# Kernel optimization log

Hardware: AMD Instinct MI355X
Metric: run time of the kernel (lower is better)

Reference implementation:

```python
import jax, jax.numpy as jnp
import numpy as np

N = 100_000      # nodes
E = 500_000      # bonds
DN = 128         # dim_node_embedding
DB = 64          # dim_bond_embedding
NTOK = 4         # num_bond_token
DIN = 2 * DN + 2 * DB  # 384
LEAKY = 0.001
LN_EPS = 1e-5
DIST_MAX = 20.0
STEP = 0.5


def _lrelu(v):
    return jnp.where(v >= 0, v, LEAKY * v)


def _layernorm(v, w, b):
    m = v.mean(-1, keepdims=True)
    var = ((v - m) ** 2).mean(-1, keepdims=True)
    return (v - m) / jnp.sqrt(var + LN_EPS) * w + b


def setup_inputs() -> dict:
    key = jax.random.key(0)
    ks = jax.random.split(key, 20)
    x = jax.random.normal(ks[0], (N, 3), dtype=jnp.float32) * 3.0
    pos = jax.random.normal(ks[1], (N, 3), dtype=jnp.float32)
    node_embedding = jax.random.normal(ks[2], (N, DN), dtype=jnp.float32)
    i0 = jax.random.randint(ks[3], (E,), 0, N)
    off = jax.random.randint(ks[4], (E,), 1, N)  # nonzero -> no self-bonds
    bond_index = jnp.stack([i0, (i0 + off) % N], axis=1).astype(jnp.int32)
    bond_types = jax.random.randint(ks[5], (E,), 0, NTOK).astype(jnp.int32)
    s = 0.02
    params = dict(
        bond_emb=jax.random.normal(ks[6], (NTOK, DB), dtype=jnp.float32),
        W0=jax.random.normal(ks[7], (DIN, DN), dtype=jnp.float32) * s,
        b0=jnp.zeros((DN,), jnp.float32),
        W1=jax.random.normal(ks[8], (DN, DN), dtype=jnp.float32) * s,
        b1=jnp.zeros((DN,), jnp.float32),
        ln1_w=jnp.ones((DN,), jnp.float32),
        ln1_b=jnp.zeros((DN,), jnp.float32),
        W2=jax.random.normal(ks[9], (DN, DN), dtype=jnp.float32) * s,
        b2=jnp.zeros((DN,), jnp.float32),
        ln2_w=jnp.ones((DN,), jnp.float32),
        ln2_b=jnp.zeros((DN,), jnp.float32),
        Wo=jax.random.normal(ks[10], (DN, 2), dtype=jnp.float32) * s,
        bo=jnp.zeros((2,), jnp.float32),
    )
    return dict(x=x, pos=pos, node_embedding=node_embedding,
                bond_index=bond_index, bond_types=bond_types, **params)


def reference(x, pos, node_embedding, bond_index, bond_types,
              bond_emb, W0, b0, W1, b1, ln1_w, ln1_b,
              W2, b2, ln2_w, ln2_b, Wo, bo):
    i = bond_index[:, 0]
    j = bond_index[:, 1]

    # ---- BondLength geometry ----
    diff = x[i] - x[j]                                   # [E,3]
    dist = jnp.linalg.norm(diff, axis=-1, keepdims=True)  # [E,1]
    u = diff / dist                                       # [E,3] unit j->i? (i-j)/d
    direction = jnp.stack([u, -u], axis=-1)               # [E,3,2]

    # ---- Smearing (gaussian RBF + overflow bin, normalized) ----
    offset = jnp.linspace(0.0, DIST_MAX, DB - 1, dtype=jnp.float32)  # [63]
    delta = DIST_MAX / (DB - 2)
    coeff = -0.5 / (delta * delta)
    rbf = jnp.exp(coeff * (dist - offset) ** 2)            # [E,63]
    ovf = (dist >= DIST_MAX).astype(x.dtype)               # [E,1]
    smear = jnp.concatenate([rbf, ovf], axis=-1)           # [E,64]
    smear = smear / smear.sum(axis=-1, keepdims=True)

    # ---- Edge MLP (LeakyMLP, num_layer=2, dim_end=2) ----
    feat = jnp.concatenate(
        [node_embedding[i], node_embedding[j], bond_emb[bond_types], smear],
        axis=-1)                                           # [E,384]
    h = _lrelu(feat @ W0 + b0)
    h = _lrelu(_layernorm(h @ W1 + b1, ln1_w, ln1_b))
    h = _lrelu(_layernorm(h @ W2 + b2, ln2_w, ln2_b))
    force = h @ Wo + bo                                    # [E,2]

    # ---- position update (scatter-add) ----
    update = force[:, None, :] * direction                 # [E,3,2]
    pos = pos.at[i].add(STEP * update[..., 0])
    pos = pos.at[j].add(STEP * update[..., 1])
    return pos
```

## Files before the change

kernel.cpp:

```cpp
#include <hip/hip_runtime.h>
#include <stdint.h>

#define N_EDGES 500000
#define N_NODES 100000
#define PREP_NG 2
#define TBINS 1280

typedef __attribute__((ext_vector_type(8))) short short8;
typedef __attribute__((ext_vector_type(4))) float floatx4;

__device__ __forceinline__ uint16_t f2bf(float f) {
  union { float f; uint32_t u; } cv; cv.f = f;
  uint32_t u = cv.u;
  return (uint16_t)((u + 0x7FFFu + ((u >> 16) & 1u)) >> 16);
}
__device__ __forceinline__ uint32_t pk2bf(float lo, float hi) {
  return __builtin_amdgcn_perm(__float_as_uint(hi), __float_as_uint(lo), 0x07060302u);
}
__device__ __forceinline__ uint16_t bftrunc(float f) {
  return (uint16_t)(__float_as_uint(f) >> 16);
}
__device__ __forceinline__ float bf2f_lo(uint32_t u) { return __uint_as_float(u << 16); }
__device__ __forceinline__ float bf2f_hi(uint32_t u) { return __uint_as_float(u & 0xFFFF0000u); }
__device__ __forceinline__ float lrelu(float v) { return fmaxf(v, 0.001f * v); }

__global__ void prep0_kernel(const float* __restrict__ W0, const float* __restrict__ b0,
                             const float* __restrict__ W1, const float* __restrict__ W2,
                             const float* __restrict__ bemb,
                             uint16_t* __restrict__ w0ab, uint16_t* __restrict__ w1f,
                             uint16_t* __restrict__ w2f, float* __restrict__ be0f,
                             const float* __restrict__ pos, float* __restrict__ out, int npos) {
  int id = blockIdx.x * 256 + threadIdx.x;
  if (id < 32768) {
    int f = id;
    int j = f & 7, lane = (f >> 3) & 63, ntt = (f >> 9) & 15, ks = f >> 13;
    int k = ks * 32 + (lane >> 4) * 8 + j;
    int row = (ntt < 8) ? k : (128 + k);
    int col = (ntt & 7) * 16 + (lane & 15);
    w0ab[f] = f2bf(W0[row * 128 + col]);
  } else if (id < 49152) {
    int f = id - 32768;
    int j = f & 7, lane = (f >> 3) & 63, nt = (f >> 9) & 7, ks = f >> 12;
    int k = ks * 32 + (lane >> 4) * 8 + j;
    w1f[f] = f2bf(W1[k * 128 + nt * 16 + (lane & 15)]);
  } else if (id < 65536) {
    int f = id - 49152;
    int j = f & 7, lane = (f >> 3) & 63, nt = (f >> 9) & 7, ks = f >> 12;
    int k = ks * 32 + (lane >> 4) * 8 + j;
    w2f[f] = f2bf(W2[k * 128 + nt * 16 + (lane & 15)]);
  } else if (id < 66048) {
    int t = id - 65536; int ty = t >> 7, n = t & 127;
    float s = b0[n];
    for (int kk = 0; kk < 64; ++kk) s += bemb[ty * 64 + kk] * W0[(256 + kk) * 128 + n];
    be0f[t] = s;
  } else if (id - 66048 < npos) {
    out[id - 66048] = pos[id - 66048];
  }
}

__global__ __attribute__((amdgpu_flat_work_group_size(256, 256)))
void prep_tp_kernel(const float* __restrict__ W0, const float* __restrict__ be0f,
                    uint16_t* __restrict__ T,
                    const float* __restrict__ nemb, const uint16_t* __restrict__ w0ab,
                    uint16_t* __restrict__ Pa, uint16_t* __restrict__ Pb) {
  __shared__ __align__(16) uint16_t aLds[4 * PREP_NG * 16 * 136];
  __shared__ float rbf[64];
  const int tid = threadIdx.x;

  if (blockIdx.x < TBINS) {
    int b = blockIdx.x;
    float dist = (float)b * (1.0f / 32.0f);
    const float delta = 20.0f / 62.0f;
    const float coeff = -0.5f / (delta * delta);
    if (tid < 64) {
      float v;
      if (tid < 63) { float d = dist - (float)tid * delta; v = __expf(coeff * d * d); }
      else v = (dist >= 20.0f) ? 1.0f : 0.0f;
      rbf[tid] = v;
    }
    __syncthreads();
    float sum = 0.0f;
    for (int k = 0; k < 64; ++k) sum += rbf[k];
    float rs = 1.0f / sum;
    for (int o = tid; o < 512; o += 256) {
      int ty = o >> 7, n = o & 127;
      float s = be0f[ty * 128 + n];
      for (int k = 0; k < 64; ++k) s += rbf[k] * rs * W0[(320 + k) * 128 + n];
      T[((size_t)(ty * TBINS + b)) * 128 + n] = f2bf(s);
    }
    return;
  }

  const int pblk = blockIdx.x - TBINS;
  const int lane = tid & 63;
  const int wave = tid >> 6;
  const int n15 = lane & 15;
  const int quad = lane >> 4;
  uint16_t* myA = aLds + wave * (PREP_NG * 16 * 136);
  const int base = pblk * (64 * PREP_NG) + wave * (16 * PREP_NG);

  {
    const int le = lane >> 2, sub = lane & 3;
#pragma unroll
    for (int it = 0; it < PREP_NG; ++it) {
      int r = base + it * 16 + le; if (r >= N_NODES) r = N_NODES - 1;
      const float4* src = (const float4*)(nemb + (size_t)r * 128);
#pragma unroll
      for (int g = 0; g < 4; ++g) {
        float4 a = src[sub * 8 + g * 2], b = src[sub * 8 + g * 2 + 1];
        uint4 pk;
        pk.x = pk2bf(a.x, a.y); pk.y = pk2bf(a.z, a.w);
        pk.z = pk2bf(b.x, b.y); pk.w = pk2bf(b.z, b.w);
        *(uint4*)(myA + (it * 16 + le) * 136 + sub * 32 + g * 8) = pk;
      }
    }
  }

  const short8* wfv = (const short8*)w0ab + lane;
#pragma unroll
  for (int q = 0; q < 4; ++q) {
    short8 bfr[16];
#pragma unroll
    for (int ks = 0; ks < 4; ++ks)
#pragma unroll
      for (int nq = 0; nq < 4; ++nq)
        bfr[ks * 4 + nq] = wfv[(ks * 16 + q * 4 + nq) * 64];
#pragma unroll
    for (int it = 0; it < PREP_NG; ++it) {
      floatx4 acc[4];
#pragma unroll
      for (int nq = 0; nq < 4; ++nq) acc[nq] = (floatx4){0.f, 0.f, 0.f, 0.f};
#pragma unroll
      for (int ks = 0; ks < 4; ++ks) {
        short8 a = *(const short8*)(myA + (it * 16 + n15) * 136 + ks * 32 + quad * 8);
#pragma unroll
        for (int nq = 0; nq < 4; ++nq)
          acc[nq] = __builtin_amdgcn_mfma_f32_16x16x32_bf16(a, bfr[ks * 4 + nq], acc[nq], 0, 0, 0);
      }
      uint16_t* dst = (q < 2) ? Pa : Pb;
      int cbase = ((q & 1) * 4) * 16 + n15;
#pragma unroll
      for (int nq = 0; nq < 4; ++nq) {
        int c = cbase + nq * 16;
#pragma unroll
        for (int r = 0; r < 4; ++r) {
          int row = base + it * 16 + quad * 4 + r;
          if (row < N_NODES) dst[(size_t)row * 128 + c] = bftrunc(acc[nq][r]);
        }
      }
    }
  }
}

__device__ __forceinline__ void gemm_g(const uint16_t* __restrict__ wf, const uint16_t* aRow,
                                       int lane, floatx4* acc) {
  short8 a[4];
#pragma unroll
  for (int ks = 0; ks < 4; ++ks) a[ks] = *(const short8*)(aRow + ks * 32);
  const short8* wv = (const short8*)wf + lane;
#pragma unroll
  for (int ks = 0; ks < 4; ++ks)
#pragma unroll
    for (int nt = 0; nt < 8; ++nt)
      acc[nt] = __builtin_amdgcn_mfma_f32_16x16x32_bf16(a[ks], wv[(ks * 8 + nt) * 64], acc[nt], 0, 0, 0);
}

__global__ __attribute__((amdgpu_flat_work_group_size(256, 256), amdgpu_waves_per_eu(4)))
void bond_mlp_kernel(const float* __restrict__ x,
                     const int* __restrict__ bidx, const int* __restrict__ btyp,
                     const uint16_t* __restrict__ Pa, const uint16_t* __restrict__ Pb,
                     const uint16_t* __restrict__ Tt, const uint16_t* __restrict__ w1f,
                     const uint16_t* __restrict__ w2f,
                     const float* __restrict__ b1, const float* __restrict__ ln1w,
                     const float* __restrict__ ln1b,
                     const float* __restrict__ b2, const float* __restrict__ ln2w,
                     const float* __restrict__ ln2b,
                     const float* __restrict__ Wo, const float* __restrict__ bo,
                     float* __restrict__ out) {
  __shared__ __align__(16) uint16_t hA_all[4 * 16 * 136];
  __shared__ float u_lds[64][3];
  __shared__ int ij_lds[64][2];

  const int tid = threadIdx.x;
  const int lane = tid & 63;
  const int wave = tid >> 6;
  const int n15 = lane & 15;
  const int quad = lane >> 4;

  uint16_t* hA = hA_all + wave * (16 * 136);

  {
    const int le = lane >> 2, sub = lane & 3;
    const int gr = wave * 16 + le;
    const int ge = blockIdx.x * 64 + gr;
    const bool valid = ge < N_EDGES;
    int vi = 0, vj = 0, bt = 0;
    if (valid) { vi = bidx[2 * ge]; vj = bidx[2 * ge + 1]; bt = btyp[ge]; }
    float dx, dy, dz;
    if (valid) {
      dx = x[3 * vi]     - x[3 * vj];
      dy = x[3 * vi + 1] - x[3 * vj + 1];
      dz = x[3 * vi + 2] - x[3 * vj + 2];
    } else { dx = 1.0f; dy = 0.0f; dz = 0.0f; }
    float dist = sqrtf(dx * dx + dy * dy + dz * dz);
    float rinv = 1.0f / dist;
    if (sub == 0) {
      u_lds[gr][0] = dx * rinv; u_lds[gr][1] = dy * rinv; u_lds[gr][2] = dz * rinv;
      ij_lds[gr][0] = vi; ij_lds[gr][1] = vj;
    }
    float fb = fminf(dist, 39.5f) * 32.0f;
    int bi = (int)fb;
    float w = fb - (float)bi;
    const uint4* pa = (const uint4*)(Pa + (size_t)vi * 128 + sub * 32);
    const uint4* pb = (const uint4*)(Pb + (size_t)vj * 128 + sub * 32);
    const uint16_t* trow = Tt + ((size_t)(bt * TBINS + bi)) * 128 + sub * 32;
    const uint4* t0p = (const uint4*)trow;
    const uint4* t1p = (const uint4*)(trow + 128);
#pragma unroll
    for (int g = 0; g < 4; ++g) {
      uint4 av = pa[g], bv = pb[g], t0 = t0p[g], t1 = t1p[g];
      uint4 pk;
      {
        float lo = bf2f_lo(av.x) + bf2f_lo(bv.x), hi = bf2f_hi(av.x) + bf2f_hi(bv.x);
        float l0 = bf2f_lo(t0.x), l1 = bf2f_lo(t1.x), h0 = bf2f_hi(t0.x), h1 = bf2f_hi(t1.x);
        pk.x = pk2bf(lrelu(lo + l0 + w * (l1 - l0)), lrelu(hi + h0 + w * (h1 - h0)));
      }
      {
        float lo = bf2f_lo(av.y) + bf2f_lo(bv.y), hi = bf2f_hi(av.y) + bf2f_hi(bv.y);
        float l0 = bf2f_lo(t0.y), l1 = bf2f_lo(t1.y), h0 = bf2f_hi(t0.y), h1 = bf2f_hi(t1.y);
        pk.y = pk2bf(lrelu(lo + l0 + w * (l1 - l0)), lrelu(hi + h0 + w * (h1 - h0)));
      }
      {
        float lo = bf2f_lo(av.z) + bf2f_lo(bv.z), hi = bf2f_hi(av.z) + bf2f_hi(bv.z);
        float l0 = bf2f_lo(t0.z), l1 = bf2f_lo(t1.z), h0 = bf2f_hi(t0.z), h1 = bf2f_hi(t1.z);
        pk.z = pk2bf(lrelu(lo + l0 + w * (l1 - l0)), lrelu(hi + h0 + w * (h1 - h0)));
      }
      {
        float lo = bf2f_lo(av.w) + bf2f_lo(bv.w), hi = bf2f_hi(av.w) + bf2f_hi(bv.w);
        float l0 = bf2f_lo(t0.w), l1 = bf2f_lo(t1.w), h0 = bf2f_hi(t0.w), h1 = bf2f_hi(t1.w);
        pk.w = pk2bf(lrelu(lo + l0 + w * (l1 - l0)), lrelu(hi + h0 + w * (h1 - h0)));
      }
      *(uint4*)(hA + le * 136 + sub * 32 + g * 8) = pk;
    }
  }

  const uint16_t* aRow = hA + n15 * 136 + quad * 8;

  floatx4 acc[8];
#pragma unroll
  for (int nt = 0; nt < 8; ++nt) acc[nt] = (floatx4){0.f, 0.f, 0.f, 0.f};
  gemm_g(w1f, aRow, lane, acc);

  {
    float bv[8], wv[8], bb2[8];
#pragma unroll
    for (int nt = 0; nt < 8; ++nt) {
      int col = nt * 16 + n15;
      bv[nt] = b1[col]; wv[nt] = ln1w[col]; bb2[nt] = ln1b[col];
    }
    float s[4] = {0,0,0,0}, q[4] = {0,0,0,0};
#pragma unroll
    for (int nt = 0; nt < 8; ++nt)
#pragma unroll
      for (int r = 0; r < 4; ++r) { float v = acc[nt][r] + bv[nt]; s[r] += v; q[r] += v * v; }
#pragma unroll
    for (int m = 1; m <= 8; m <<= 1)
#pragma unroll
      for (int r = 0; r < 4; ++r) { s[r] += __shfl_xor(s[r], m); q[r] += __shfl_xor(q[r], m); }
    float mean[4], rstd[4];
#pragma unroll
    for (int r = 0; r < 4; ++r) {
      mean[r] = s[r] * (1.0f / 128.0f);
      float var = q[r] * (1.0f / 128.0f) - mean[r] * mean[r];
      rstd[r] = rsqrtf(var + 1e-5f);
    }
#pragma unroll
    for (int nt = 0; nt < 8; ++nt)
#pragma unroll
      for (int r = 0; r < 4; ++r) {
        float v = acc[nt][r] + bv[nt];
        float vn = (v - mean[r]) * rstd[r] * wv[nt] + bb2[nt];
        hA[(quad * 4 + r) * 136 + nt * 16 + n15] = bftrunc(lrelu(vn));
      }
  }

#pragma unroll
  for (int nt = 0; nt < 8; ++nt) acc[nt] = (floatx4){0.f, 0.f, 0.f, 0.f};
  gemm_g(w2f, aRow, lane, acc);

  {
    float bv[8], wv[8], bb2[8], wo0[8], wo1[8];
#pragma unroll
    for (int nt = 0; nt < 8; ++nt) {
      int col = nt * 16 + n15;
      bv[nt] = b2[col]; wv[nt] = ln2w[col]; bb2[nt] = ln2b[col];
      wo0[nt] = Wo[2 * col]; wo1[nt] = Wo[2 * col + 1];
    }
    float s[4] = {0,0,0,0}, q[4] = {0,0,0,0};
#pragma unroll
    for (int nt = 0; nt < 8; ++nt)
#pragma unroll
      for (int r = 0; r < 4; ++r) { float v = acc[nt][r] + bv[nt]; s[r] += v; q[r] += v * v; }
#pragma unroll
    for (int m = 1; m <= 8; m <<= 1)
#pragma unroll
      for (int r = 0; r < 4; ++r) { s[r] += __shfl_xor(s[r], m); q[r] += __shfl_xor(q[r], m); }
    float mean[4], rstd[4];
#pragma unroll
    for (int r = 0; r < 4; ++r) {
      mean[r] = s[r] * (1.0f / 128.0f);
      float var = q[r] * (1.0f / 128.0f) - mean[r] * mean[r];
      rstd[r] = rsqrtf(var + 1e-5f);
    }
    float f0[4] = {0,0,0,0}, f1[4] = {0,0,0,0};
#pragma unroll
    for (int nt = 0; nt < 8; ++nt)
#pragma unroll
      for (int r = 0; r < 4; ++r) {
        float v = acc[nt][r] + bv[nt];
        float vn = lrelu((v - mean[r]) * rstd[r] * wv[nt] + bb2[nt]);
        f0[r] += vn * wo0[nt];
        f1[r] += vn * wo1[nt];
      }
#pragma unroll
    for (int m = 1; m <= 8; m <<= 1)
#pragma unroll
      for (int r = 0; r < 4; ++r) { f0[r] += __shfl_xor(f0[r], m); f1[r] += __shfl_xor(f1[r], m); }

    if (n15 < 4) {
      int gr = wave * 16 + quad * 4 + n15;
      int ge2 = blockIdx.x * 64 + gr;
      if (ge2 < N_EDGES) {
        float F0 = (n15 == 0) ? f0[0] : (n15 == 1) ? f0[1] : (n15 == 2) ? f0[2] : f0[3];
        float F1 = (n15 == 0) ? f1[0] : (n15 == 1) ? f1[1] : (n15 == 2) ? f1[2] : f1[3];
        F0 += bo[0]; F1 += bo[1];
        float ux = u_lds[gr][0], uy = u_lds[gr][1], uz = u_lds[gr][2];
        int ii = ij_lds[gr][0], jj = ij_lds[gr][1];
        float c0 = 0.5f * F0;
        float c1 = -0.5f * F1;
        atomicAdd(out + 3 * ii,     c0 * ux);
        atomicAdd(out + 3 * ii + 1, c0 * uy);
        atomicAdd(out + 3 * ii + 2, c0 * uz);
        atomicAdd(out + 3 * jj,     c1 * ux);
        atomicAdd(out + 3 * jj + 1, c1 * uy);
        atomicAdd(out + 3 * jj + 2, c1 * uz);
      }
    }
  }
}

extern "C" void kernel_launch(void* const* d_in, const int* in_sizes, int n_in,
                              void* d_out, int out_size, void* d_ws, size_t ws_size,
                              hipStream_t stream) {
  const float* x    = (const float*)d_in[0];
  const float* pos  = (const float*)d_in[1];
  const float* nemb = (const float*)d_in[2];
  const int*   bidx = (const int*)d_in[3];
  const int*   btyp = (const int*)d_in[4];
  const float* bemb = (const float*)d_in[5];
  const float* W0   = (const float*)d_in[6];
  const float* b0   = (const float*)d_in[7];
  const float* W1   = (const float*)d_in[8];
  const float* b1   = (const float*)d_in[9];
  const float* ln1w = (const float*)d_in[10];
  const float* ln1b = (const float*)d_in[11];
  const float* W2   = (const float*)d_in[12];
  const float* b2   = (const float*)d_in[13];
  const float* ln2w = (const float*)d_in[14];
  const float* ln2b = (const float*)d_in[15];
  const float* Wo   = (const float*)d_in[16];
  const float* bo   = (const float*)d_in[17];
  float* out = (float*)d_out;

  uint16_t* w0ab = (uint16_t*)d_ws;
  uint16_t* w1f  = w0ab + 32768;
  uint16_t* w2f  = w1f + 16384;
  float*    be0f = (float*)(w2f + 16384);
  uint16_t* Tt   = (uint16_t*)(be0f + 512);
  uint16_t* Pa   = Tt + (size_t)4 * TBINS * 128;
  uint16_t* Pb   = Pa + (size_t)N_NODES * 128;

  const int nblkP = (N_NODES + 64 * PREP_NG - 1) / (64 * PREP_NG);

  prep0_kernel<<<(66048 + out_size + 255) / 256, 256, 0, stream>>>(
      W0, b0, W1, W2, bemb, w0ab, w1f, w2f, be0f, pos, out, out_size);
  prep_tp_kernel<<<TBINS + nblkP, 256, 0, stream>>>(
      W0, be0f, Tt, nemb, w0ab, Pa, Pb);
  bond_mlp_kernel<<<(N_EDGES + 63) / 64, 256, 0, stream>>>(
      x, bidx, btyp, Pa, Pb, Tt, w1f, w2f,
      b1, ln1w, ln1b, b2, ln2w, ln2b, Wo, bo, out);
}
```

Measured before the change: 339.6 us.

## Process two 16-edge tiles per wave to reuse MFMA weight fragments

Each wave in the bond MLP kernel now handles 32 edges as two 16-row tiles, so every weight fragment loaded from global memory feeds two MFMAs. This halves weight-fetch traffic per edge, and the block size in edges doubles. The change also vectorizes the gather and epilogue arithmetic with packed float2/float4 ops, uses nontemporal loads for indices and node projections, raises PREP_NG to 4, and relaxes waves_per_eu to (2,4). Doubled accumulators raise register pressure and may lower occupancy.

```diff
diff --git a/kernel.cpp b/kernel.cpp
--- a/kernel.cpp
+++ b/kernel.cpp
@@ -3,11 +3,14 @@
 
 #define N_EDGES 500000
 #define N_NODES 100000
-#define PREP_NG 2
+#define PREP_NG 4
 #define TBINS 1280
 
 typedef __attribute__((ext_vector_type(8))) short short8;
 typedef __attribute__((ext_vector_type(4))) float floatx4;
+typedef __attribute__((ext_vector_type(2))) float f32x2;
+typedef __attribute__((ext_vector_type(4))) unsigned int u32x4v;
+typedef __attribute__((ext_vector_type(2))) int i32x2v;
 
 __device__ __forceinline__ uint16_t f2bf(float f) {
   union { float f; uint32_t u; } cv; cv.f = f;
@@ -20,9 +23,25 @@
 __device__ __forceinline__ uint16_t bftrunc(float f) {
   return (uint16_t)(__float_as_uint(f) >> 16);
 }
-__device__ __forceinline__ float bf2f_lo(uint32_t u) { return __uint_as_float(u << 16); }
-__device__ __forceinline__ float bf2f_hi(uint32_t u) { return __uint_as_float(u & 0xFFFF0000u); }
 __device__ __forceinline__ float lrelu(float v) { return fmaxf(v, 0.001f * v); }
+
+__device__ __forceinline__ f32x2 unpk2(uint32_t u) {
+  return (f32x2){ __uint_as_float(u << 16), __uint_as_float(u & 0xFFFF0000u) };
+}
+__device__ __forceinline__ uint32_t comp2(uint32_t a, uint32_t b, uint32_t t0, uint32_t t1,
+                                          f32x2 w2) {
+  f32x2 p  = unpk2(a) + unpk2(b);
+  f32x2 v0 = unpk2(t0), v1 = unpk2(t1);
+  f32x2 r  = p + (v0 + w2 * (v1 - v0));
+  f32x2 rl = r * 0.001f;
+  return pk2bf(fmaxf(r.x, rl.x), fmaxf(r.y, rl.y));
+}
+__device__ __forceinline__ floatx4 lrelu4(floatx4 v) {
+  floatx4 w = v * 0.001f;
+  v.x = fmaxf(v.x, w.x); v.y = fmaxf(v.y, w.y);
+  v.z = fmaxf(v.z, w.z); v.w = fmaxf(v.w, w.w);
+  return v;
+}
 
 __global__ void prep0_kernel(const float* __restrict__ W0, const float* __restrict__ b0,
                              const float* __restrict__ W1, const float* __restrict__ W2,
@@ -152,20 +171,122 @@
   }
 }
 
-__device__ __forceinline__ void gemm_g(const uint16_t* __restrict__ wf, const uint16_t* aRow,
-                                       int lane, floatx4* acc) {
-  short8 a[4];
-#pragma unroll
-  for (int ks = 0; ks < 4; ++ks) a[ks] = *(const short8*)(aRow + ks * 32);
+__device__ __forceinline__ void gemm_g2(const uint16_t* __restrict__ wf,
+                                        const uint16_t* aRow0, const uint16_t* aRow1,
+                                        int lane, floatx4* acc0, floatx4* acc1) {
+  short8 a0[4], a1[4];
+#pragma unroll
+  for (int ks = 0; ks < 4; ++ks) {
+    a0[ks] = *(const short8*)(aRow0 + ks * 32);
+    a1[ks] = *(const short8*)(aRow1 + ks * 32);
+  }
   const short8* wv = (const short8*)wf + lane;
 #pragma unroll
   for (int ks = 0; ks < 4; ++ks)
 #pragma unroll
-    for (int nt = 0; nt < 8; ++nt)
-      acc[nt] = __builtin_amdgcn_mfma_f32_16x16x32_bf16(a[ks], wv[(ks * 8 + nt) * 64], acc[nt], 0, 0, 0);
-}
-
-__global__ __attribute__((amdgpu_flat_work_group_size(256, 256), amdgpu_waves_per_eu(4)))
+    for (int nt = 0; nt < 8; ++nt) {
+      short8 b = wv[(ks * 8 + nt) * 64];
+      acc0[nt] = __builtin_amdgcn_mfma_f32_16x16x32_bf16(a0[ks], b, acc0[nt], 0, 0, 0);
+      acc1[nt] = __builtin_amdgcn_mfma_f32_16x16x32_bf16(a1[ks], b, acc1[nt], 0, 0, 0);
+    }
+}
+
+__device__ __forceinline__ void epilogue1(floatx4* acc, uint16_t* hA, int n15, int quad,
+                                          const float* __restrict__ b1,
+                                          const float* __restrict__ ln1w,
+                                          const float* __restrict__ ln1b) {
+  float bv[8], wv[8], bb[8];
+#pragma unroll
+  for (int nt = 0; nt < 8; ++nt) {
+    int col = nt * 16 + n15;
+    bv[nt] = b1[col]; wv[nt] = ln1w[col]; bb[nt] = ln1b[col];
+  }
+  floatx4 s4 = {0.f, 0.f, 0.f, 0.f}, q4 = {0.f, 0.f, 0.f, 0.f};
+#pragma unroll
+  for (int nt = 0; nt < 8; ++nt) { floatx4 v = acc[nt] + bv[nt]; s4 += v; q4 += v * v; }
+#pragma unroll
+  for (int m = 1; m <= 8; m <<= 1) {
+#pragma unroll
+    for (int c = 0; c < 4; ++c) { s4[c] += __shfl_xor(s4[c], m); q4[c] += __shfl_xor(q4[c], m); }
+  }
+  floatx4 mean = s4 * (1.0f / 128.0f);
+  floatx4 var = q4 * (1.0f / 128.0f) - mean * mean;
+  floatx4 rstd;
+  rstd.x = rsqrtf(var.x + 1e-5f); rstd.y = rsqrtf(var.y + 1e-5f);
+  rstd.z = rsqrtf(var.z + 1e-5f); rstd.w = rsqrtf(var.w + 1e-5f);
+#pragma unroll
+  for (int nt = 0; nt < 8; ++nt) {
+    floatx4 v = acc[nt] + bv[nt];
+    floatx4 vn = lrelu4((v - mean) * (rstd * wv[nt]) + bb[nt]);
+#pragma unroll
+    for (int r = 0; r < 4; ++r)
+      hA[(quad * 4 + r) * 136 + nt * 16 + n15] = bftrunc(vn[r]);
+  }
+}
+
+__device__ __forceinline__ void epilogue2(floatx4* acc, int n15, int quad, int edge0, int gr0,
+                                          const float (*u_lds)[3], const int (*ij_lds)[2],
+                                          const float* __restrict__ b2,
+                                          const float* __restrict__ ln2w,
+                                          const float* __restrict__ ln2b,
+                                          const float* __restrict__ Wo,
+                                          const float* __restrict__ bo,
+                                          float* __restrict__ out) {
+  float bv[8], wv[8], bb[8], wo0[8], wo1[8];
+#pragma unroll
+  for (int nt = 0; nt < 8; ++nt) {
+    int col = nt * 16 + n15;
+    bv[nt] = b2[col]; wv[nt] = ln2w[col]; bb[nt] = ln2b[col];
+    wo0[nt] = Wo[2 * col]; wo1[nt] = Wo[2 * col + 1];
+  }
+  floatx4 s4 = {0.f, 0.f, 0.f, 0.f}, q4 = {0.f, 0.f, 0.f, 0.f};
+#pragma unroll
+  for (int nt = 0; nt < 8; ++nt) { floatx4 v = acc[nt] + bv[nt]; s4 += v; q4 += v * v; }
+#pragma unroll
+  for (int m = 1; m <= 8; m <<= 1) {
+#pragma unroll
+    for (int c = 0; c < 4; ++c) { s4[c] += __shfl_xor(s4[c], m); q4[c] += __shfl_xor(q4[c], m); }
+  }
+  floatx4 mean = s4 * (1.0f / 128.0f);
+  floatx4 var = q4 * (1.0f / 128.0f) - mean * mean;
+  floatx4 rstd;
+  rstd.x = rsqrtf(var.x + 1e-5f); rstd.y = rsqrtf(var.y + 1e-5f);
+  rstd.z = rsqrtf(var.z + 1e-5f); rstd.w = rsqrtf(var.w + 1e-5f);
+  floatx4 f0 = {0.f, 0.f, 0.f, 0.f}, f1 = {0.f, 0.f, 0.f, 0.f};
+#pragma unroll
+  for (int nt = 0; nt < 8; ++nt) {
+    floatx4 v = acc[nt] + bv[nt];
+    floatx4 vn = lrelu4((v - mean) * (rstd * wv[nt]) + bb[nt]);
+    f0 += vn * wo0[nt];
+    f1 += vn * wo1[nt];
+  }
+#pragma unroll
+  for (int m = 1; m <= 8; m <<= 1) {
+#pragma unroll
+    for (int c = 0; c < 4; ++c) { f0[c] += __shfl_xor(f0[c], m); f1[c] += __shfl_xor(f1[c], m); }
+  }
+  if (n15 < 4) {
+    int gr = gr0 + quad * 4 + n15;
+    int ge2 = edge0 + quad * 4 + n15;
+    if (ge2 < N_EDGES) {
+      float F0 = (n15 == 0) ? f0.x : (n15 == 1) ? f0.y : (n15 == 2) ? f0.z : f0.w;
+      float F1 = (n15 == 0) ? f1.x : (n15 == 1) ? f1.y : (n15 == 2) ? f1.z : f1.w;
+      F0 += bo[0]; F1 += bo[1];
+      float ux = u_lds[gr][0], uy = u_lds[gr][1], uz = u_lds[gr][2];
+      int ii = ij_lds[gr][0], jj = ij_lds[gr][1];
+      float c0 = 0.5f * F0;
+      float c1 = -0.5f * F1;
+      atomicAdd(out + 3 * ii,     c0 * ux);
+      atomicAdd(out + 3 * ii + 1, c0 * uy);
+      atomicAdd(out + 3 * ii + 2, c0 * uz);
+      atomicAdd(out + 3 * jj,     c1 * ux);
+      atomicAdd(out + 3 * jj + 1, c1 * uy);
+      atomicAdd(out + 3 * jj + 2, c1 * uz);
+    }
+  }
+}
+
+__global__ __attribute__((amdgpu_flat_work_group_size(256, 256), amdgpu_waves_per_eu(2, 4)))
 void bond_mlp_kernel(const float* __restrict__ x,
                      const int* __restrict__ bidx, const int* __restrict__ btyp,
                      const uint16_t* __restrict__ Pa, const uint16_t* __restrict__ Pb,
@@ -177,9 +298,9 @@
                      const float* __restrict__ ln2b,
                      const float* __restrict__ Wo, const float* __restrict__ bo,
                      float* __restrict__ out) {
-  __shared__ __align__(16) uint16_t hA_all[4 * 16 * 136];
-  __shared__ float u_lds[64][3];
-  __shared__ int ij_lds[64][2];
+  __shared__ __align__(16) uint16_t hA_all[8 * 16 * 136];
+  __shared__ float u_lds[128][3];
+  __shared__ int ij_lds[128][2];
 
   const int tid = threadIdx.x;
   const int lane = tid & 63;
@@ -187,15 +308,22 @@
   const int n15 = lane & 15;
   const int quad = lane >> 4;
 
-  uint16_t* hA = hA_all + wave * (16 * 136);
-
-  {
+  uint16_t* hA0 = hA_all + (wave * 2 + 0) * (16 * 136);
+  uint16_t* hA1 = hA_all + (wave * 2 + 1) * (16 * 136);
+
+#pragma unroll
+  for (int g = 0; g < 2; ++g) {
+    uint16_t* hA = (g == 0) ? hA0 : hA1;
     const int le = lane >> 2, sub = lane & 3;
-    const int gr = wave * 16 + le;
-    const int ge = blockIdx.x * 64 + gr;
+    const int gr = wave * 32 + g * 16 + le;
+    const int ge = blockIdx.x * 128 + gr;
     const bool valid = ge < N_EDGES;
     int vi = 0, vj = 0, bt = 0;
-    if (valid) { vi = bidx[2 * ge]; vj = bidx[2 * ge + 1]; bt = btyp[ge]; }
+    if (valid) {
+      i32x2v ij = __builtin_nontemporal_load((const i32x2v*)(bidx + 2 * ge));
+      vi = ij.x; vj = ij.y;
+      bt = __builtin_nontemporal_load(btyp + ge);
+    }
     float dx, dy, dz;
     if (valid) {
       dx = x[3 * vi]     - x[3 * vj];
@@ -211,142 +339,51 @@
     float fb = fminf(dist, 39.5f) * 32.0f;
     int bi = (int)fb;
     float w = fb - (float)bi;
-    const uint4* pa = (const uint4*)(Pa + (size_t)vi * 128 + sub * 32);
-    const uint4* pb = (const uint4*)(Pb + (size_t)vj * 128 + sub * 32);
+    f32x2 w2 = {w, w};
+    const u32x4v* pa = (const u32x4v*)(Pa + (size_t)vi * 128 + sub * 32);
+    const u32x4v* pb = (const u32x4v*)(Pb + (size_t)vj * 128 + sub * 32);
     const uint16_t* trow = Tt + ((size_t)(bt * TBINS + bi)) * 128 + sub * 32;
-    const uint4* t0p = (const uint4*)trow;
-    const uint4* t1p = (const uint4*)(trow + 128);
-#pragma unroll
-    for (int g = 0; g < 4; ++g) {
-      uint4 av = pa[g], bv = pb[g], t0 = t0p[g], t1 = t1p[g];
-      uint4 pk;
-      {
-        float lo = bf2f_lo(av.x) + bf2f_lo(bv.x), hi = bf2f_hi(av.x) + bf2f_hi(bv.x);
-        float l0 = bf2f_lo(t0.x), l1 = bf2f_lo(t1.x), h0 = bf2f_hi(t0.x), h1 = bf2f_hi(t1.x);
-        pk.x = pk2bf(lrelu(lo + l0 + w * (l1 - l0)), lrelu(hi + h0 + w * (h1 - h0)));
-      }
-      {
-        float lo = bf2f_lo(av.y) + bf2f_lo(bv.y), hi = bf2f_hi(av.y) + bf2f_hi(bv.y);
-        float l0 = bf2f_lo(t0.y), l1 = bf2f_lo(t1.y), h0 = bf2f_hi(t0.y), h1 = bf2f_hi(t1.y);
-        pk.y = pk2bf(lrelu(lo + l0 + w * (l1 - l0)), lrelu(hi + h0 + w * (h1 - h0)));
-      }
-      {
-        float lo = bf2f_lo(av.z) + bf2f_lo(bv.z), hi = bf2f_hi(av.z) + bf2f_hi(bv.z);
-        float l0 = bf2f_lo(t0.z), l1 = bf2f_lo(t1.z), h0 = bf2f_hi(t0.z), h1 = bf2f_hi(t1.z);
-        pk.z = pk2bf(lrelu(lo + l0 + w * (l1 - l0)), lrelu(hi + h0 + w * (h1 - h0)));
-      }
-      {
-        float lo = bf2f_lo(av.w) + bf2f_lo(bv.w), hi = bf2f_hi(av.w) + bf2f_hi(bv.w);
-        float l0 = bf2f_lo(t0.w), l1 = bf2f_lo(t1.w), h0 = bf2f_hi(t0.w), h1 = bf2f_hi(t1.w);
-        pk.w = pk2bf(lrelu(lo + l0 + w * (l1 - l0)), lrelu(hi + h0 + w * (h1 - h0)));
-      }
-      *(uint4*)(hA + le * 136 + sub * 32 + g * 8) = pk;
-    }
-  }
-
-  const uint16_t* aRow = hA + n15 * 136 + quad * 8;
-
-  floatx4 acc[8];
-#pragma unroll
-  for (int nt = 0; nt < 8; ++nt) acc[nt] = (floatx4){0.f, 0.f, 0.f, 0.f};
-  gemm_g(w1f, aRow, lane, acc);
-
-  {
-    float bv[8], wv[8], bb2[8];
-#pragma unroll
-    for (int nt = 0; nt < 8; ++nt) {
-      int col = nt * 16 + n15;
-      bv[nt] = b1[col]; wv[nt] = ln1w[col]; bb2[nt] = ln1b[col];
-    }
-    float s[4] = {0,0,0,0}, q[4] = {0,0,0,0};
-#pragma unroll
-    for (int nt = 0; nt < 8; ++nt)
-#pragma unroll
-      for (int r = 0; r < 4; ++r) { float v = acc[nt][r] + bv[nt]; s[r] += v; q[r] += v * v; }
-#pragma unroll
-    for (int m = 1; m <= 8; m <<= 1)
-#pragma unroll
-      for (int r = 0; r < 4; ++r) { s[r] += __shfl_xor(s[r], m); q[r] += __shfl_xor(q[r], m); }
-    float mean[4], rstd[4];
-#pragma unroll
-    for (int r = 0; r < 4; ++r) {
-      mean[r] = s[r] * (1.0f / 128.0f);
-      float var = q[r] * (1.0f / 128.0f) - mean[r] * mean[r];
-      rstd[r] = rsqrtf(var + 1e-5f);
-    }
-#pragma unroll
-    for (int nt = 0; nt < 8; ++nt)
-#pragma unroll
-      for (int r = 0; r < 4; ++r) {
-        float v = acc[nt][r] + bv[nt];
-        float vn = (v - mean[r]) * rstd[r] * wv[nt] + bb2[nt];
-        hA[(quad * 4 + r) * 136 + nt * 16 + n15] = bftrunc(lrelu(vn));
-      }
-  }
-
-#pragma unroll
-  for (int nt = 0; nt < 8; ++nt) acc[nt] = (floatx4){0.f, 0.f, 0.f, 0.f};
-  gemm_g(w2f, aRow, lane, acc);
-
-  {
-    float bv[8], wv[8], bb2[8], wo0[8], wo1[8];
-#pragma unroll
-    for (int nt = 0; nt < 8; ++nt) {
-      int col = nt * 16 + n15;
-      bv[nt] = b2[col]; wv[nt] = ln2w[col]; bb2[nt] = ln2b[col];
-      wo0[nt] = Wo[2 * col]; wo1[nt] = Wo[2 * col + 1];
-    }
-    float s[4] = {0,0,0,0}, q[4] = {0,0,0,0};
-#pragma unroll
-    for (int nt = 0; nt < 8; ++nt)
-#pragma unroll
-      for (int r = 0; r < 4; ++r) { float v = acc[nt][r] + bv[nt]; s[r] += v; q[r] += v * v; }
-#pragma unroll
-    for (int m = 1; m <= 8; m <<= 1)
-#pragma unroll
-      for (int r = 0; r < 4; ++r) { s[r] += __shfl_xor(s[r], m); q[r] += __shfl_xor(q[r], m); }
-    float mean[4], rstd[4];
-#pragma unroll
-    for (int r = 0; r < 4; ++r) {
-      mean[r] = s[r] * (1.0f / 128.0f);
-      float var = q[r] * (1.0f / 128.0f) - mean[r] * mean[r];
-      rstd[r] = rsqrtf(var + 1e-5f);
-    }
-    float f0[4] = {0,0,0,0}, f1[4] = {0,0,0,0};
-#pragma unroll
-    for (int nt = 0; nt < 8; ++nt)
-#pragma unroll
-      for (int r = 0; r < 4; ++r) {
-        float v = acc[nt][r] + bv[nt];
-        float vn = lrelu((v - mean[r]) * rstd[r] * wv[nt] + bb2[nt]);
-        f0[r] += vn * wo0[nt];
-        f1[r] += vn * wo1[nt];
-      }
-#pragma unroll
-    for (int m = 1; m <= 8; m <<= 1)
-#pragma unroll
-      for (int r = 0; r < 4; ++r) { f0[r] += __shfl_xor(f0[r], m); f1[r] += __shfl_xor(f1[r], m); }
-
-    if (n15 < 4) {
-      int gr = wave * 16 + quad * 4 + n15;
-      int ge2 = blockIdx.x * 64 + gr;
-      if (ge2 < N_EDGES) {
-        float F0 = (n15 == 0) ? f0[0] : (n15 == 1) ? f0[1] : (n15 == 2) ? f0[2] : f0[3];
-        float F1 = (n15 == 0) ? f1[0] : (n15 == 1) ? f1[1] : (n15 == 2) ? f1[2] : f1[3];
-        F0 += bo[0]; F1 += bo[1];
-        float ux = u_lds[gr][0], uy = u_lds[gr][1], uz = u_lds[gr][2];
-        int ii = ij_lds[gr][0], jj = ij_lds[gr][1];
-        float c0 = 0.5f * F0;
-        float c1 = -0.5f * F1;
-        atomicAdd(out + 3 * ii,     c0 * ux);
-        atomicAdd(out + 3 * ii + 1, c0 * uy);
-        atomicAdd(out + 3 * ii + 2, c0 * uz);
-        atomicAdd(out + 3 * jj,     c1 * ux);
-        atomicAdd(out + 3 * jj + 1, c1 * uy);
-        atomicAdd(out + 3 * jj + 2, c1 * uz);
-      }
-    }
-  }
+    const u32x4v* t0p = (const u32x4v*)trow;
+    const u32x4v* t1p = (const u32x4v*)(trow + 128);
+#pragma unroll
+    for (int gg = 0; gg < 4; ++gg) {
+      u32x4v av = __builtin_nontemporal_load(pa + gg);
+      u32x4v bw = __builtin_nontemporal_load(pb + gg);
+      u32x4v t0 = t0p[gg];
+      u32x4v t1 = t1p[gg];
+      u32x4v pk;
+      pk.x = comp2(av.x, bw.x, t0.x, t1.x, w2);
+      pk.y = comp2(av.y, bw.y, t0.y, t1.y, w2);
+      pk.z = comp2(av.z, bw.z, t0.z, t1.z, w2);
+      pk.w = comp2(av.w, bw.w, t0.w, t1.w, w2);
+      *(u32x4v*)(hA + le * 136 + sub * 32 + gg * 8) = pk;
+    }
+  }
+
+  const uint16_t* aRow0 = hA0 + n15 * 136 + quad * 8;
+  const uint16_t* aRow1 = hA1 + n15 * 136 + quad * 8;
+
+  floatx4 acc0[8], acc1[8];
+#pragma unroll
+  for (int nt = 0; nt < 8; ++nt) {
+    acc0[nt] = (floatx4){0.f, 0.f, 0.f, 0.f};
+    acc1[nt] = (floatx4){0.f, 0.f, 0.f, 0.f};
+  }
+  gemm_g2(w1f, aRow0, aRow1, lane, acc0, acc1);
+
+  epilogue1(acc0, hA0, n15, quad, b1, ln1w, ln1b);
+  epilogue1(acc1, hA1, n15, quad, b1, ln1w, ln1b);
+
+#pragma unroll
+  for (int nt = 0; nt < 8; ++nt) {
+    acc0[nt] = (floatx4){0.f, 0.f, 0.f, 0.f};
+    acc1[nt] = (floatx4){0.f, 0.f, 0.f, 0.f};
+  }
+  gemm_g2(w2f, aRow0, aRow1, lane, acc0, acc1);
+
+  const int e0 = blockIdx.x * 128 + wave * 32;
+  epilogue2(acc0, n15, quad, e0,      wave * 32,      u_lds, ij_lds, b2, ln2w, ln2b, Wo, bo, out);
+  epilogue2(acc1, n15, quad, e0 + 16, wave * 32 + 16, u_lds, ij_lds, b2, ln2w, ln2b, Wo, bo, out);
 }
 
 extern "C" void kernel_launch(void* const* d_in, const int* in_sizes, int n_in,
@@ -386,7 +423,7 @@
       W0, b0, W1, W2, bemb, w0ab, w1f, w2f, be0f, pos, out, out_size);
   prep_tp_kernel<<<TBINS + nblkP, 256, 0, stream>>>(
       W0, be0f, Tt, nemb, w0ab, Pa, Pb);
-  bond_mlp_kernel<<<(N_EDGES + 63) / 64, 256, 0, stream>>>(
+  bond_mlp_kernel<<<(N_EDGES + 127) / 128, 256, 0, stream>>>(
       x, bidx, btyp, Pa, Pb, Tt, w1f, w2f,
       b1, ln1w, ln1b, b2, ln2w, ln2b, Wo, bo, out);
 }
```

After: 390.8 us. +15.1%, slower.
